# Performance work log

Measured on AMD Instinct MI355X. Metric: run time of the kernel, lower is better.

The kernel has to match this reference:

```python
import jax, jax.numpy as jnp
import numpy as np

N, D, H, K = 131072, 512, 128, 3
NPOS, NNEG = 8192, 8192
KM_ITERS = 4
PROTO_SHIFT = 0.15
PROTO_LOGIT_SCALE = 0.2
TEMP = 2.5


def _sq_cdist(x, c):
    # squared euclidean distance, matches torch.cdist(...).pow(2)
    d = jnp.sum(x * x, -1, keepdims=True) + jnp.sum(c * c, -1)[None, :] - 2.0 * (x @ c.T)
    return jnp.maximum(d, 0.0)


def _kmeans(x, k, iters):
    # torch.linspace(0, n-1, steps=k).long() init, fixed iteration count
    n = x.shape[0]
    idx = jnp.linspace(0.0, n - 1, k).astype(jnp.int32)
    centers = x[idx]
    for _ in range(iters):
        assign = jnp.argmin(_sq_cdist(x, centers), axis=1)
        sums = jax.ops.segment_sum(x, assign, num_segments=k)
        counts = jax.ops.segment_sum(jnp.ones((n,), x.dtype), assign, num_segments=k)[:, None]
        # empty cluster keeps old center (mask.any() branch in torch)
        centers = jnp.where(counts > 0, sums / jnp.maximum(counts, 1.0), centers)
    return centers


def setup_inputs() -> dict:
    key = jax.random.key(0)
    ks = jax.random.split(key, 10)
    s = 1.0 / np.sqrt(D).astype(np.float32)
    return {
        "z_cls": jax.random.normal(ks[0], (N, D), jnp.float32),
        "z_proto": jax.random.normal(ks[1], (N, D), jnp.float32),
        "pos_ctx": jax.random.normal(ks[2], (D,), jnp.float32),
        "neg_ctx": jax.random.normal(ks[3], (D,), jnp.float32),
        "W1": jax.random.normal(ks[4], (H, D), jnp.float32) * s,
        "b1": jnp.zeros((H,), jnp.float32),
        "W2": jax.random.normal(ks[5], (1, H), jnp.float32) * (1.0 / np.sqrt(H).astype(np.float32)),
        "b2": jnp.zeros((1,), jnp.float32),
        "Wp": jax.random.normal(ks[6], (D, D), jnp.float32) * s,
        "bp": jnp.zeros((D,), jnp.float32),
        "Wn": jax.random.normal(ks[7], (D, D), jnp.float32) * s,
        "bn": jnp.zeros((D,), jnp.float32),
        "pos_idx": jax.random.randint(ks[8], (NPOS,), 0, N),
        "neg_idx": jax.random.randint(ks[9], (NNEG,), 0, N),
    }


def reference(z_cls, z_proto, pos_ctx, neg_ctx, W1, b1, W2, b2, Wp, bp, Wn, bn, pos_idx, neg_idx):
    # _build_prototypes (pos_idx/neg_idx nonempty path)
    pos_proto = _kmeans(z_proto[pos_idx], K, KM_ITERS)          # [K, D]
    neg_proto = jnp.mean(z_proto[neg_idx], axis=0)              # [D]
    # _calibrate (ema not initialized -> no EMA blend)
    pos_proto = pos_proto + PROTO_SHIFT * (pos_ctx @ Wp.T + bp)[None, :]
    neg_proto = neg_proto + PROTO_SHIFT * (neg_ctx @ Wn.T + bn)
    # distances
    d_pos_all = _sq_cdist(z_proto, pos_proto)                   # [N, K]
    d_pos = jnp.min(d_pos_all, axis=1)
    pos_assign = jnp.argmin(d_pos_all, axis=1)
    d_neg = jnp.mean((z_proto - neg_proto[None, :]) ** 2, axis=1)
    proto_logit = (d_neg - d_pos) / np.sqrt(D).astype(np.float32)
    # cls head (eval mode: dropout is identity)
    h = jax.nn.relu(z_cls @ W1.T + b1)
    cls_logit = (h @ W2.T + b2)[:, 0]
    logits = (cls_logit + PROTO_LOGIT_SCALE * proto_logit) / TEMP
    prob = jax.nn.sigmoid(logits)
    return (logits, prob, PROTO_LOGIT_SCALE * proto_logit, pos_assign, d_pos_all, pos_proto, neg_proto)
```

## Files before the change

kernel.cpp:

```cpp
#include <hip/hip_runtime.h>
#include <hip/hip_bf16.h>

#define NPTS 131072
#define DIM  512
#define HID  128
#define KCL  3
#define NPOSI 8192
#define NNEGI 8192

typedef __attribute__((ext_vector_type(8))) short bf16x8;
typedef __attribute__((ext_vector_type(4))) float f32x4;

enum {
  WS_SHIFT_POS = 0,
  WS_SHIFT_NEG = 512,
  WS_NEGSUM    = 1024,
  WS_NEGPART   = 1536,
  WS_SUMS      = 132608,
  WS_PPROTO    = 138764,
  WS_PN        = 140812,
  WS_W1FRAG    = 140816,
  WS_CLSL      = 173584,
};
#define SUMS_STRIDE 1539

__device__ __forceinline__ short f2bf(float x) {
  __hip_bfloat16 h = __float2bfloat16(x);
  return *reinterpret_cast<short*>(&h);
}

__global__ __launch_bounds__(256) void k_prep(const float* __restrict__ W1,
                                              const float* __restrict__ Wp, const float* __restrict__ bp,
                                              const float* __restrict__ Wn, const float* __restrict__ bn,
                                              const float* __restrict__ pos_ctx, const float* __restrict__ neg_ctx,
                                              const float* __restrict__ zp, const int* __restrict__ neg_idx,
                                              float* __restrict__ ws) {
  int bid = blockIdx.x, t = threadIdx.x;
  if (bid < 32) {
    int fid = bid * 256 + t;
    int kc = fid >> 9;
    int n  = (fid >> 6) & 7;
    int l  = fid & 63;
    int row = n * 16 + (l & 15);
    int col = kc * 32 + (l >> 4) * 8;
    const float* src = W1 + (size_t)row * DIM + col;
    float4 v0 = *(const float4*)(src);
    float4 v1 = *(const float4*)(src + 4);
    bf16x8 f;
    f[0] = f2bf(v0.x); f[1] = f2bf(v0.y); f[2] = f2bf(v0.z); f[3] = f2bf(v0.w);
    f[4] = f2bf(v1.x); f[5] = f2bf(v1.y); f[6] = f2bf(v1.z); f[7] = f2bf(v1.w);
    ((bf16x8*)(ws + WS_W1FRAG))[fid] = f;
  } else if (bid < 64) {
    int b = bid - 32;
    int mat = b >> 4;
    const float* W    = mat ? Wn : Wp;
    const float* bias = mat ? bn : bp;
    const float* ctx  = mat ? neg_ctx : pos_ctx;
    float* outp = ws + (mat ? WS_SHIFT_NEG : WS_SHIFT_POS);
    int row = (b & 15) * 32 + (t >> 3);
    int sub = t & 7;
    const float* wr = W + row * DIM + sub * 64;
    const float* cr = ctx + sub * 64;
    float s = 0.f;
#pragma unroll
    for (int j = 0; j < 64; j += 4) {
      float4 w4 = *(const float4*)(wr + j);
      float4 c4 = *(const float4*)(cr + j);
      s += w4.x * c4.x + w4.y * c4.y + w4.z * c4.z + w4.w * c4.w;
    }
    s += __shfl_xor(s, 1);
    s += __shfl_xor(s, 2);
    s += __shfl_xor(s, 4);
    if (sub == 0) outp[row] = 0.15f * (s + bias[row]);
  } else if (bid < 320) {
    int jb = bid - 64;
    int c0 = t * 2;
    float a0 = 0.f, a1 = 0.f;
    int base = jb * 32;
#pragma unroll 4
    for (int jj = 0; jj < 32; ++jj) {
      int row = neg_idx[base + jj];
      float2 v = *(const float2*)(zp + (size_t)row * DIM + c0);
      a0 += v.x; a1 += v.y;
    }
    ws[WS_NEGPART + jb * DIM + c0]     = a0;
    ws[WS_NEGPART + jb * DIM + c0 + 1] = a1;
  } else {
    for (int idx = t; idx < 4 * SUMS_STRIDE; idx += 256) ws[WS_SUMS + idx] = 0.f;
  }
}

template <int IT>
__global__ __launch_bounds__(256) void k_km(const float* __restrict__ zp,
                                            const int* __restrict__ pos_idx,
                                            float* __restrict__ ws) {
  int bid = blockIdx.x, t = threadIdx.x;
  if (IT == 0 && bid == 256) {
    int c0 = t * 2;
    float a0 = 0.f, a1 = 0.f;
#pragma unroll 8
    for (int j = 0; j < 256; ++j) {
      float2 v = *(const float2*)(ws + WS_NEGPART + j * DIM + c0);
      a0 += v.x; a1 += v.y;
    }
    ws[WS_NEGSUM + c0]     = a0;
    ws[WS_NEGSUM + c0 + 1] = a1;
    return;
  }
  __shared__ float cc[KCL * DIM];
  __shared__ float cn[KCL];
  __shared__ float lsum[KCL * DIM];
  __shared__ float lcnt[KCL];
  int w = t >> 6, l = t & 63;

  for (int idx = t; idx < KCL * DIM; idx += 256) lsum[idx] = 0.f;
  if (t < KCL) lcnt[t] = 0.f;

  for (int idx = t; idx < KCL * DIM; idx += 256) {
    int k = idx >> 9;
    int sel = (k == 0) ? 0 : ((k == 1) ? 4095 : 8191);
    float v = zp[(size_t)pos_idx[sel] * DIM + (idx & 511)];
#pragma unroll
    for (int j = 0; j < IT; ++j) {
      float cntv = ws[WS_SUMS + j * SUMS_STRIDE + 3 * DIM + k];
      float sv   = ws[WS_SUMS + j * SUMS_STRIDE + idx];
      v = (cntv > 0.f) ? sv / cntv : v;
    }
    cc[idx] = v;
  }
  __syncthreads();
  if (w < KCL) {
    float s = 0.f;
#pragma unroll
    for (int m = 0; m < 8; ++m) { float v = cc[w * DIM + l + m * 64]; s += v * v; }
#pragma unroll
    for (int m = 1; m < 64; m <<= 1) s += __shfl_xor(s, m);
    if (l == 0) cn[w] = s;
  }
  __syncthreads();

  float ck0[8], ck1[8], ck2[8];
#pragma unroll
  for (int j = 0; j < 8; ++j) {
    ck0[j] = cc[0 * DIM + l * 8 + j];
    ck1[j] = cc[1 * DIM + l * 8 + j];
    ck2[j] = cc[2 * DIM + l * 8 + j];
  }
  float cn0 = cn[0], cn1 = cn[1], cn2 = cn[2];
  float acc0[8] = {0,0,0,0,0,0,0,0}, acc1[8] = {0,0,0,0,0,0,0,0}, acc2[8] = {0,0,0,0,0,0,0,0};
  float cnt0 = 0.f, cnt1 = 0.f, cnt2 = 0.f;

  int wid = bid * 4 + w;
#pragma unroll 2
  for (int p = wid; p < NPOSI; p += 1024) {
    int row = pos_idx[p];
    const float* xr = zp + (size_t)row * DIM + l * 8;
    float4 x0 = *(const float4*)(xr);
    float4 x1 = *(const float4*)(xr + 4);
    float x[8] = {x0.x, x0.y, x0.z, x0.w, x1.x, x1.y, x1.z, x1.w};
    float d0 = 0.f, d1 = 0.f, d2 = 0.f;
#pragma unroll
    for (int j = 0; j < 8; ++j) { d0 += x[j] * ck0[j]; d1 += x[j] * ck1[j]; d2 += x[j] * ck2[j]; }
#pragma unroll
    for (int m = 1; m < 64; m <<= 1) {
      d0 += __shfl_xor(d0, m); d1 += __shfl_xor(d1, m); d2 += __shfl_xor(d2, m);
    }
    float t0 = cn0 - 2.f * d0, t1 = cn1 - 2.f * d1, t2 = cn2 - 2.f * d2;
    int a = 0; float best = t0;
    if (t1 < best) { best = t1; a = 1; }
    if (t2 < best) { best = t2; a = 2; }
    if (a == 0)      { cnt0 += 1.f;
#pragma unroll
      for (int j = 0; j < 8; ++j) acc0[j] += x[j]; }
    else if (a == 1) { cnt1 += 1.f;
#pragma unroll
      for (int j = 0; j < 8; ++j) acc1[j] += x[j]; }
    else             { cnt2 += 1.f;
#pragma unroll
      for (int j = 0; j < 8; ++j) acc2[j] += x[j]; }
  }
#pragma unroll
  for (int j = 0; j < 8; ++j) {
    atomicAdd(&lsum[0 * DIM + l * 8 + j], acc0[j]);
    atomicAdd(&lsum[1 * DIM + l * 8 + j], acc1[j]);
    atomicAdd(&lsum[2 * DIM + l * 8 + j], acc2[j]);
  }
  if (l == 0) {
    atomicAdd(&lcnt[0], cnt0); atomicAdd(&lcnt[1], cnt1); atomicAdd(&lcnt[2], cnt2);
  }
  __syncthreads();
  for (int idx = t; idx < KCL * DIM; idx += 256) atomicAdd(&ws[WS_SUMS + IT * SUMS_STRIDE + idx], lsum[idx]);
  if (t < KCL) atomicAdd(&ws[WS_SUMS + IT * SUMS_STRIDE + 3 * DIM + t], lcnt[t]);
}

__global__ __launch_bounds__(256) void k_fin(const float* __restrict__ zp,
                                             const int* __restrict__ pos_idx,
                                             float* __restrict__ ws,
                                             float* __restrict__ out) {
  __shared__ __align__(16) float pp[4 * DIM];
  int t = threadIdx.x, w = t >> 6, l = t & 63;
  for (int idx = t; idx < KCL * DIM; idx += 256) {
    int k = idx >> 9, d = idx & 511;
    int sel = (k == 0) ? 0 : ((k == 1) ? 4095 : 8191);
    float v = zp[(size_t)pos_idx[sel] * DIM + d];
#pragma unroll
    for (int j = 0; j < 4; ++j) {
      float cntv = ws[WS_SUMS + j * SUMS_STRIDE + 3 * DIM + k];
      float sv   = ws[WS_SUMS + j * SUMS_STRIDE + idx];
      v = (cntv > 0.f) ? sv / cntv : v;
    }
    pp[idx] = v + ws[WS_SHIFT_POS + d];
  }
  for (int d = t; d < DIM; d += 256)
    pp[3 * DIM + d] = ws[WS_NEGSUM + d] * (1.f / NNEGI) + ws[WS_SHIFT_NEG + d];
  __syncthreads();
  {
    float s = 0.f;
#pragma unroll
    for (int m = 0; m < 8; ++m) { float v = pp[w * DIM + l + m * 64]; s += v * v; }
#pragma unroll
    for (int m = 1; m < 64; m <<= 1) s += __shfl_xor(s, m);
    if (l == 0) ws[WS_PN + w] = s;
  }
  for (int idx = t; idx < 4 * DIM; idx += 256) {
    ws[WS_PPROTO + idx] = pp[idx];
    out[7 * NPTS + idx] = pp[idx];
  }
}

__global__ __launch_bounds__(256, 2) void k_cls(const float* __restrict__ zc,
                                                const float* __restrict__ b1,
                                                const float* __restrict__ W2,
                                                const float* __restrict__ b2,
                                                float* __restrict__ ws) {
  int t = threadIdx.x, w = t >> 6, l = t & 63;
  int i0 = blockIdx.x * 64;
  const bf16x8* w1f = (const bf16x8*)(ws + WS_W1FRAG);
  int arow = i0 + w * 16 + (l & 15);
  const float* aptr = zc + (size_t)arow * DIM + (l >> 4) * 8;

  f32x4 acc[8];
#pragma unroll
  for (int n = 0; n < 8; ++n) acc[n] = (f32x4){0.f, 0.f, 0.f, 0.f};

  float4 A[3][2];
  bf16x8 B[2][8];
#pragma unroll
  for (int s = 0; s < 3; ++s) {
    A[s][0] = *(const float4*)(aptr + s * 32);
    A[s][1] = *(const float4*)(aptr + s * 32 + 4);
  }
#pragma unroll
  for (int n = 0; n < 8; ++n) B[0][n] = w1f[n * 64 + l];

#pragma unroll
  for (int kc = 0; kc < 16; ++kc) {
    float4 a0 = A[kc % 3][0], a1 = A[kc % 3][1];
    bf16x8 af;
    af[0] = f2bf(a0.x); af[1] = f2bf(a0.y); af[2] = f2bf(a0.z); af[3] = f2bf(a0.w);
    af[4] = f2bf(a1.x); af[5] = f2bf(a1.y); af[6] = f2bf(a1.z); af[7] = f2bf(a1.w);
    if (kc + 3 < 16) {
      A[kc % 3][0] = *(const float4*)(aptr + (kc + 3) * 32);
      A[kc % 3][1] = *(const float4*)(aptr + (kc + 3) * 32 + 4);
    }
    if (kc + 1 < 16) {
#pragma unroll
      for (int n = 0; n < 8; ++n) B[(kc + 1) & 1][n] = w1f[(kc + 1) * 512 + n * 64 + l];
    }
#pragma unroll
    for (int n = 0; n < 8; ++n)
      acc[n] = __builtin_amdgcn_mfma_f32_16x16x32_bf16(af, B[kc & 1][n], acc[n], 0, 0, 0);
  }

  float p[4] = {0.f, 0.f, 0.f, 0.f};
  int col_l = l & 15;
#pragma unroll
  for (int n = 0; n < 8; ++n) {
    int col = n * 16 + col_l;
    float bb = b1[col], w2v = W2[col];
#pragma unroll
    for (int r = 0; r < 4; ++r) {
      float h = acc[n][r] + bb;
      h = h > 0.f ? h : 0.f;
      p[r] += h * w2v;
    }
  }
#pragma unroll
  for (int m = 1; m < 16; m <<= 1) {
#pragma unroll
    for (int r = 0; r < 4; ++r) p[r] += __shfl_xor(p[r], m);
  }
  if (col_l == 0) {
    float b2v = b2[0];
    int rbase = i0 + w * 16 + (l >> 4) * 4;
#pragma unroll
    for (int r = 0; r < 4; ++r) ws[WS_CLSL + rbase + r] = p[r] + b2v;
  }
}

__global__ __launch_bounds__(256, 4) void k_proto(const float* __restrict__ zp,
                                                  const float* __restrict__ ws,
                                                  float* __restrict__ out) {
  __shared__ __align__(16) float pp[4 * DIM];
  __shared__ float pns[4];
  int t = threadIdx.x;
  for (int idx = t; idx < 4 * DIM; idx += 256) pp[idx] = ws[WS_PPROTO + idx];
  if (t < 4) pns[t] = ws[WS_PN + t];
  __syncthreads();

  int w = t >> 6, l = t & 63, s = l & 7, r = l >> 3;
  int i = blockIdx.x * 32 + w * 8 + r;
  const float* xr = zp + (size_t)i * DIM;

  float d0 = 0.f, d1 = 0.f, d2 = 0.f, dn = 0.f, sx = 0.f;
#pragma unroll
  for (int j = 0; j < 16; ++j) {
    int col = j * 32 + s * 4;
    float4 x  = *(const float4*)(xr + col);
    float4 c0 = *(const float4*)(&pp[0 * DIM + col]);
    float4 c1 = *(const float4*)(&pp[1 * DIM + col]);
    float4 c2 = *(const float4*)(&pp[2 * DIM + col]);
    float4 c3 = *(const float4*)(&pp[3 * DIM + col]);
    d0 += x.x * c0.x + x.y * c0.y + x.z * c0.z + x.w * c0.w;
    d1 += x.x * c1.x + x.y * c1.y + x.z * c1.z + x.w * c1.w;
    d2 += x.x * c2.x + x.y * c2.y + x.z * c2.z + x.w * c2.w;
    dn += x.x * c3.x + x.y * c3.y + x.z * c3.z + x.w * c3.w;
    sx += x.x * x.x  + x.y * x.y  + x.z * x.z  + x.w * x.w;
  }
#pragma unroll
  for (int m = 1; m < 8; m <<= 1) {
    d0 += __shfl_xor(d0, m);
    d1 += __shfl_xor(d1, m);
    d2 += __shfl_xor(d2, m);
    dn += __shfl_xor(dn, m);
    sx += __shfl_xor(sx, m);
  }
  if (s == 0) {
    float e0 = sx + pns[0] - 2.f * d0; e0 = fmaxf(e0, 0.f);
    float e1 = sx + pns[1] - 2.f * d1; e1 = fmaxf(e1, 0.f);
    float e2 = sx + pns[2] - 2.f * d2; e2 = fmaxf(e2, 0.f);
    float dpos = e0; int a = 0;
    if (e1 < dpos) { dpos = e1; a = 1; }
    if (e2 < dpos) { dpos = e2; a = 2; }
    float dneg = (sx + pns[3] - 2.f * dn) * (1.f / DIM);
    float plog = (dneg - dpos) * 0.04419417382415922f;
    float o2 = 0.2f * plog;
    float lg = (ws[WS_CLSL + i] + o2) * 0.4f;
    float prob = 1.f / (1.f + expf(-lg));
    out[i]            = lg;
    out[NPTS + i]     = prob;
    out[2 * NPTS + i] = o2;
    out[3 * NPTS + i] = (float)a;
    out[4 * NPTS + 3 * i]     = e0;
    out[4 * NPTS + 3 * i + 1] = e1;
    out[4 * NPTS + 3 * i + 2] = e2;
  }
}

extern "C" void kernel_launch(void* const* d_in, const int* in_sizes, int n_in,
                              void* d_out, int out_size, void* d_ws, size_t ws_size,
                              hipStream_t stream) {
  const float* z_cls   = (const float*)d_in[0];
  const float* z_proto = (const float*)d_in[1];
  const float* pos_ctx = (const float*)d_in[2];
  const float* neg_ctx = (const float*)d_in[3];
  const float* W1      = (const float*)d_in[4];
  const float* b1      = (const float*)d_in[5];
  const float* W2      = (const float*)d_in[6];
  const float* b2      = (const float*)d_in[7];
  const float* Wp      = (const float*)d_in[8];
  const float* bp      = (const float*)d_in[9];
  const float* Wn      = (const float*)d_in[10];
  const float* bn      = (const float*)d_in[11];
  const int* pos_idx   = (const int*)d_in[12];
  const int* neg_idx   = (const int*)d_in[13];
  float* out           = (float*)d_out;
  float* ws            = (float*)d_ws;

  k_prep<<<321, 256, 0, stream>>>(W1, Wp, bp, Wn, bn, pos_ctx, neg_ctx, z_proto, neg_idx, ws);
  k_km<0><<<257, 256, 0, stream>>>(z_proto, pos_idx, ws);
  k_km<1><<<256, 256, 0, stream>>>(z_proto, pos_idx, ws);
  k_km<2><<<256, 256, 0, stream>>>(z_proto, pos_idx, ws);
  k_km<3><<<256, 256, 0, stream>>>(z_proto, pos_idx, ws);
  k_fin<<<1, 256, 0, stream>>>(z_proto, pos_idx, ws, out);
  k_cls<<<NPTS / 64, 256, 0, stream>>>(z_cls, b1, W2, b2, ws);
  k_proto<<<NPTS / 32, 256, 0, stream>>>(z_proto, ws, out);
}
```

Baseline: 276.1 us.

## Fuse cls head with proto distances and pre-gather positive rows for kmeans

The cls MLP head and the prototype distance kernel are merged into one kernel. It stages z_cls and then z_proto tiles into LDS with async global-to-LDS loads and a swizzled layout, and keeps cls logits in shared memory instead of a workspace round trip. The positive-index rows are gathered once into a contiguous workspace buffer in the prep kernel, so each kmeans iteration reads them contiguously with 4 rows per wave over 512 blocks instead of doing indirect gathers. This removes a kernel launch and the cls-logit global traffic. In exchange it adds an extra 16 MB gather copy and a larger LDS footprint that may lower occupancy.

```diff
diff --git a/kernel.cpp b/kernel.cpp
--- a/kernel.cpp
+++ b/kernel.cpp
@@ -10,6 +10,9 @@
 
 typedef __attribute__((ext_vector_type(8))) short bf16x8;
 typedef __attribute__((ext_vector_type(4))) float f32x4;
+
+#define ASG __attribute__((address_space(1)))
+#define ASL __attribute__((address_space(3)))
 
 enum {
   WS_SHIFT_POS = 0,
@@ -20,7 +23,7 @@
   WS_PPROTO    = 138764,
   WS_PN        = 140812,
   WS_W1FRAG    = 140816,
-  WS_CLSL      = 173584,
+  WS_POSG      = 173584,
 };
 #define SUMS_STRIDE 1539
 
@@ -33,7 +36,8 @@
                                               const float* __restrict__ Wp, const float* __restrict__ bp,
                                               const float* __restrict__ Wn, const float* __restrict__ bn,
                                               const float* __restrict__ pos_ctx, const float* __restrict__ neg_ctx,
-                                              const float* __restrict__ zp, const int* __restrict__ neg_idx,
+                                              const float* __restrict__ zp,
+                                              const int* __restrict__ neg_idx, const int* __restrict__ pos_idx,
                                               float* __restrict__ ws) {
   int bid = blockIdx.x, t = threadIdx.x;
   if (bid < 32) {
@@ -77,7 +81,7 @@
     int c0 = t * 2;
     float a0 = 0.f, a1 = 0.f;
     int base = jb * 32;
-#pragma unroll 4
+#pragma unroll 8
     for (int jj = 0; jj < 32; ++jj) {
       int row = neg_idx[base + jj];
       float2 v = *(const float2*)(zp + (size_t)row * DIM + c0);
@@ -85,17 +89,35 @@
     }
     ws[WS_NEGPART + jb * DIM + c0]     = a0;
     ws[WS_NEGPART + jb * DIM + c0 + 1] = a1;
+  } else if (bid < 576) {
+    int j = bid - 320;
+    int w = t >> 6, l = t & 63;
+    int row0 = j * 32 + w * 8;
+#pragma unroll
+    for (int rb = 0; rb < 8; rb += 8) {
+      float4 a[8], b[8];
+#pragma unroll
+      for (int r = 0; r < 8; ++r) {
+        const float* src = zp + (size_t)pos_idx[row0 + rb + r] * DIM + l * 8;
+        a[r] = *(const float4*)(src);
+        b[r] = *(const float4*)(src + 4);
+      }
+#pragma unroll
+      for (int r = 0; r < 8; ++r) {
+        float* dst = ws + WS_POSG + (size_t)(row0 + rb + r) * DIM + l * 8;
+        *(float4*)(dst)     = a[r];
+        *(float4*)(dst + 4) = b[r];
+      }
+    }
   } else {
     for (int idx = t; idx < 4 * SUMS_STRIDE; idx += 256) ws[WS_SUMS + idx] = 0.f;
   }
 }
 
 template <int IT>
-__global__ __launch_bounds__(256) void k_km(const float* __restrict__ zp,
-                                            const int* __restrict__ pos_idx,
-                                            float* __restrict__ ws) {
+__global__ __launch_bounds__(256, 1) void k_km(float* __restrict__ ws) {
   int bid = blockIdx.x, t = threadIdx.x;
-  if (IT == 0 && bid == 256) {
+  if (IT == 0 && bid == 512) {
     int c0 = t * 2;
     float a0 = 0.f, a1 = 0.f;
 #pragma unroll 8
@@ -119,7 +141,7 @@
   for (int idx = t; idx < KCL * DIM; idx += 256) {
     int k = idx >> 9;
     int sel = (k == 0) ? 0 : ((k == 1) ? 4095 : 8191);
-    float v = zp[(size_t)pos_idx[sel] * DIM + (idx & 511)];
+    float v = ws[WS_POSG + (size_t)sel * DIM + (idx & 511)];
 #pragma unroll
     for (int j = 0; j < IT; ++j) {
       float cntv = ws[WS_SUMS + j * SUMS_STRIDE + 3 * DIM + k];
@@ -150,14 +172,17 @@
   float acc0[8] = {0,0,0,0,0,0,0,0}, acc1[8] = {0,0,0,0,0,0,0,0}, acc2[8] = {0,0,0,0,0,0,0,0};
   float cnt0 = 0.f, cnt1 = 0.f, cnt2 = 0.f;
 
-  int wid = bid * 4 + w;
-#pragma unroll 2
-  for (int p = wid; p < NPOSI; p += 1024) {
-    int row = pos_idx[p];
-    const float* xr = zp + (size_t)row * DIM + l * 8;
-    float4 x0 = *(const float4*)(xr);
-    float4 x1 = *(const float4*)(xr + 4);
-    float x[8] = {x0.x, x0.y, x0.z, x0.w, x1.x, x1.y, x1.z, x1.w};
+  int p0 = (bid * 4 + w) * 4;
+  const float* xbase = ws + WS_POSG + (size_t)p0 * DIM + l * 8;
+  float4 xa[4], xb[4];
+#pragma unroll
+  for (int r = 0; r < 4; ++r) {
+    xa[r] = *(const float4*)(xbase + r * DIM);
+    xb[r] = *(const float4*)(xbase + r * DIM + 4);
+  }
+#pragma unroll
+  for (int r = 0; r < 4; ++r) {
+    float x[8] = {xa[r].x, xa[r].y, xa[r].z, xa[r].w, xb[r].x, xb[r].y, xb[r].z, xb[r].w};
     float d0 = 0.f, d1 = 0.f, d2 = 0.f;
 #pragma unroll
     for (int j = 0; j < 8; ++j) { d0 += x[j] * ck0[j]; d1 += x[j] * ck1[j]; d2 += x[j] * ck2[j]; }
@@ -193,16 +218,13 @@
   if (t < KCL) atomicAdd(&ws[WS_SUMS + IT * SUMS_STRIDE + 3 * DIM + t], lcnt[t]);
 }
 
-__global__ __launch_bounds__(256) void k_fin(const float* __restrict__ zp,
-                                             const int* __restrict__ pos_idx,
-                                             float* __restrict__ ws,
-                                             float* __restrict__ out) {
+__global__ __launch_bounds__(256) void k_fin(float* __restrict__ ws, float* __restrict__ out) {
   __shared__ __align__(16) float pp[4 * DIM];
   int t = threadIdx.x, w = t >> 6, l = t & 63;
   for (int idx = t; idx < KCL * DIM; idx += 256) {
     int k = idx >> 9, d = idx & 511;
     int sel = (k == 0) ? 0 : ((k == 1) ? 4095 : 8191);
-    float v = zp[(size_t)pos_idx[sel] * DIM + d];
+    float v = ws[WS_POSG + (size_t)sel * DIM + d];
 #pragma unroll
     for (int j = 0; j < 4; ++j) {
       float cntv = ws[WS_SUMS + j * SUMS_STRIDE + 3 * DIM + k];
@@ -228,132 +250,169 @@
   }
 }
 
-__global__ __launch_bounds__(256, 2) void k_cls(const float* __restrict__ zc,
-                                                const float* __restrict__ b1,
-                                                const float* __restrict__ W2,
-                                                const float* __restrict__ b2,
-                                                float* __restrict__ ws) {
-  int t = threadIdx.x, w = t >> 6, l = t & 63;
-  int i0 = blockIdx.x * 64;
-  const bf16x8* w1f = (const bf16x8*)(ws + WS_W1FRAG);
-  int arow = i0 + w * 16 + (l & 15);
-  const float* aptr = zc + (size_t)arow * DIM + (l >> 4) * 8;
-
-  f32x4 acc[8];
-#pragma unroll
-  for (int n = 0; n < 8; ++n) acc[n] = (f32x4){0.f, 0.f, 0.f, 0.f};
-
-  float4 A[3][2];
-  bf16x8 B[2][8];
-#pragma unroll
-  for (int s = 0; s < 3; ++s) {
-    A[s][0] = *(const float4*)(aptr + s * 32);
-    A[s][1] = *(const float4*)(aptr + s * 32 + 4);
-  }
-#pragma unroll
-  for (int n = 0; n < 8; ++n) B[0][n] = w1f[n * 64 + l];
-
-#pragma unroll
-  for (int kc = 0; kc < 16; ++kc) {
-    float4 a0 = A[kc % 3][0], a1 = A[kc % 3][1];
-    bf16x8 af;
-    af[0] = f2bf(a0.x); af[1] = f2bf(a0.y); af[2] = f2bf(a0.z); af[3] = f2bf(a0.w);
-    af[4] = f2bf(a1.x); af[5] = f2bf(a1.y); af[6] = f2bf(a1.z); af[7] = f2bf(a1.w);
-    if (kc + 3 < 16) {
-      A[kc % 3][0] = *(const float4*)(aptr + (kc + 3) * 32);
-      A[kc % 3][1] = *(const float4*)(aptr + (kc + 3) * 32 + 4);
-    }
-    if (kc + 1 < 16) {
-#pragma unroll
-      for (int n = 0; n < 8; ++n) B[(kc + 1) & 1][n] = w1f[(kc + 1) * 512 + n * 64 + l];
-    }
-#pragma unroll
-    for (int n = 0; n < 8; ++n)
-      acc[n] = __builtin_amdgcn_mfma_f32_16x16x32_bf16(af, B[kc & 1][n], acc[n], 0, 0, 0);
-  }
-
-  float p[4] = {0.f, 0.f, 0.f, 0.f};
-  int col_l = l & 15;
-#pragma unroll
-  for (int n = 0; n < 8; ++n) {
-    int col = n * 16 + col_l;
-    float bb = b1[col], w2v = W2[col];
-#pragma unroll
-    for (int r = 0; r < 4; ++r) {
-      float h = acc[n][r] + bb;
-      h = h > 0.f ? h : 0.f;
-      p[r] += h * w2v;
-    }
-  }
-#pragma unroll
-  for (int m = 1; m < 16; m <<= 1) {
-#pragma unroll
-    for (int r = 0; r < 4; ++r) p[r] += __shfl_xor(p[r], m);
-  }
-  if (col_l == 0) {
-    float b2v = b2[0];
-    int rbase = i0 + w * 16 + (l >> 4) * 4;
-#pragma unroll
-    for (int r = 0; r < 4; ++r) ws[WS_CLSL + rbase + r] = p[r] + b2v;
-  }
-}
-
-__global__ __launch_bounds__(256, 4) void k_proto(const float* __restrict__ zp,
+__global__ __launch_bounds__(256, 2) void k_fused(const float* __restrict__ zc,
+                                                  const float* __restrict__ zp,
+                                                  const float* __restrict__ b1,
+                                                  const float* __restrict__ W2,
+                                                  const float* __restrict__ b2,
                                                   const float* __restrict__ ws,
                                                   float* __restrict__ out) {
+  __shared__ __align__(16) float Ast[2][16 * DIM];
   __shared__ __align__(16) float pp[4 * DIM];
   __shared__ float pns[4];
-  int t = threadIdx.x;
+  __shared__ float clsv[32];
+
+  int t = threadIdx.x, w = t >> 6, l = t & 63;
+  int pr = w >> 1, hw = w & 1;
+  int i0 = blockIdx.x * 32;
+  int pairRow0 = i0 + pr * 16;
+
+  if (t < 32) clsv[t] = 0.f;
+
+  {
+    const float* gsrc = zc + (size_t)(pairRow0 + hw * 8) * DIM;
+    float* ldsb = &Ast[pr][0];
+#pragma unroll
+    for (int i = 0; i < 16; ++i) {
+      int rloc = hw * 8 + (i >> 1);
+      int c = ((i & 1) * 256) + ((l * 4) ^ ((rloc & 7) << 3));
+      const float* src = gsrc + (size_t)(i >> 1) * DIM + c;
+      float* dst = ldsb + rloc * DIM + (i & 1) * 256;
+      __builtin_amdgcn_global_load_lds((const ASG void*)src, (ASL void*)dst, 16, 0, 0);
+    }
+  }
+
   for (int idx = t; idx < 4 * DIM; idx += 256) pp[idx] = ws[WS_PPROTO + idx];
   if (t < 4) pns[t] = ws[WS_PN + t];
-  __syncthreads();
-
-  int w = t >> 6, l = t & 63, s = l & 7, r = l >> 3;
-  int i = blockIdx.x * 32 + w * 8 + r;
-  const float* xr = zp + (size_t)i * DIM;
-
-  float d0 = 0.f, d1 = 0.f, d2 = 0.f, dn = 0.f, sx = 0.f;
-#pragma unroll
-  for (int j = 0; j < 16; ++j) {
-    int col = j * 32 + s * 4;
-    float4 x  = *(const float4*)(xr + col);
-    float4 c0 = *(const float4*)(&pp[0 * DIM + col]);
-    float4 c1 = *(const float4*)(&pp[1 * DIM + col]);
-    float4 c2 = *(const float4*)(&pp[2 * DIM + col]);
-    float4 c3 = *(const float4*)(&pp[3 * DIM + col]);
-    d0 += x.x * c0.x + x.y * c0.y + x.z * c0.z + x.w * c0.w;
-    d1 += x.x * c1.x + x.y * c1.y + x.z * c1.z + x.w * c1.w;
-    d2 += x.x * c2.x + x.y * c2.y + x.z * c2.z + x.w * c2.w;
-    dn += x.x * c3.x + x.y * c3.y + x.z * c3.z + x.w * c3.w;
-    sx += x.x * x.x  + x.y * x.y  + x.z * x.z  + x.w * x.w;
-  }
-#pragma unroll
-  for (int m = 1; m < 8; m <<= 1) {
-    d0 += __shfl_xor(d0, m);
-    d1 += __shfl_xor(d1, m);
-    d2 += __shfl_xor(d2, m);
-    dn += __shfl_xor(dn, m);
-    sx += __shfl_xor(sx, m);
-  }
-  if (s == 0) {
-    float e0 = sx + pns[0] - 2.f * d0; e0 = fmaxf(e0, 0.f);
-    float e1 = sx + pns[1] - 2.f * d1; e1 = fmaxf(e1, 0.f);
-    float e2 = sx + pns[2] - 2.f * d2; e2 = fmaxf(e2, 0.f);
-    float dpos = e0; int a = 0;
-    if (e1 < dpos) { dpos = e1; a = 1; }
-    if (e2 < dpos) { dpos = e2; a = 2; }
-    float dneg = (sx + pns[3] - 2.f * dn) * (1.f / DIM);
-    float plog = (dneg - dpos) * 0.04419417382415922f;
-    float o2 = 0.2f * plog;
-    float lg = (ws[WS_CLSL + i] + o2) * 0.4f;
-    float prob = 1.f / (1.f + expf(-lg));
-    out[i]            = lg;
-    out[NPTS + i]     = prob;
-    out[2 * NPTS + i] = o2;
-    out[3 * NPTS + i] = (float)a;
-    out[4 * NPTS + 3 * i]     = e0;
-    out[4 * NPTS + 3 * i + 1] = e1;
-    out[4 * NPTS + 3 * i + 2] = e2;
+  int col_l = l & 15;
+  float b1c[4], w2c[4];
+#pragma unroll
+  for (int nn = 0; nn < 4; ++nn) {
+    int col = (hw * 4 + nn) * 16 + col_l;
+    b1c[nn] = b1[col];
+    w2c[nn] = W2[col];
+  }
+  float b2v = b2[0];
+  __syncthreads();
+
+  {
+    const bf16x8* w1f = (const bf16x8*)(ws + WS_W1FRAG);
+    const float* pl = &Ast[pr][0];
+    int sub = l >> 4, row = l & 15;
+    int swz = (row & 7) << 3;
+    int abase = row * DIM;
+    f32x4 acc[4];
+#pragma unroll
+    for (int nn = 0; nn < 4; ++nn) acc[nn] = (f32x4){0.f, 0.f, 0.f, 0.f};
+    bf16x8 B2[2][4];
+#pragma unroll
+    for (int nn = 0; nn < 4; ++nn) B2[0][nn] = w1f[(hw * 4 + nn) * 64 + l];
+
+#pragma unroll
+    for (int kc = 0; kc < 16; ++kc) {
+      int pidx = abase + ((kc * 32 + sub * 8) ^ swz);
+      float4 a0 = *(const float4*)&pl[pidx];
+      float4 a1 = *(const float4*)&pl[pidx + 4];
+      if (kc < 15) {
+#pragma unroll
+        for (int nn = 0; nn < 4; ++nn)
+          B2[(kc + 1) & 1][nn] = w1f[(kc + 1) * 512 + (hw * 4 + nn) * 64 + l];
+      }
+      bf16x8 af;
+      af[0] = f2bf(a0.x); af[1] = f2bf(a0.y); af[2] = f2bf(a0.z); af[3] = f2bf(a0.w);
+      af[4] = f2bf(a1.x); af[5] = f2bf(a1.y); af[6] = f2bf(a1.z); af[7] = f2bf(a1.w);
+#pragma unroll
+      for (int nn = 0; nn < 4; ++nn)
+        acc[nn] = __builtin_amdgcn_mfma_f32_16x16x32_bf16(af, B2[kc & 1][nn], acc[nn], 0, 0, 0);
+    }
+    float prt[4] = {0.f, 0.f, 0.f, 0.f};
+#pragma unroll
+    for (int nn = 0; nn < 4; ++nn) {
+#pragma unroll
+      for (int r = 0; r < 4; ++r) {
+        float h = acc[nn][r] + b1c[nn];
+        h = h > 0.f ? h : 0.f;
+        prt[r] += h * w2c[nn];
+      }
+    }
+#pragma unroll
+    for (int m = 1; m < 16; m <<= 1) {
+#pragma unroll
+      for (int r = 0; r < 4; ++r) prt[r] += __shfl_xor(prt[r], m);
+    }
+    if (col_l == 0) {
+      float add = hw ? 0.f : b2v;
+#pragma unroll
+      for (int r = 0; r < 4; ++r)
+        atomicAdd(&clsv[pr * 16 + sub * 4 + r], prt[r] + add);
+    }
+  }
+  __syncthreads();
+
+  {
+    const float* gsrc = zp + (size_t)(pairRow0 + hw * 8) * DIM;
+    float* ldsb = &Ast[pr][0];
+#pragma unroll
+    for (int i = 0; i < 16; ++i) {
+      int rloc = hw * 8 + (i >> 1);
+      int c = ((i & 1) * 256) + ((l * 4) ^ ((rloc & 7) << 3));
+      const float* src = gsrc + (size_t)(i >> 1) * DIM + c;
+      float* dst = ldsb + rloc * DIM + (i & 1) * 256;
+      __builtin_amdgcn_global_load_lds((const ASG void*)src, (ASL void*)dst, 16, 0, 0);
+    }
+  }
+  __syncthreads();
+
+  {
+    int s = l & 7, r8 = l >> 3;
+    const float* xl = &Ast[w >> 1][0];
+    int rloc = (w & 1) * 8 + r8;
+    int swz = (rloc & 7) << 3;
+    int xbase = rloc * DIM;
+    float d0 = 0.f, d1 = 0.f, d2 = 0.f, dn = 0.f, sx = 0.f;
+#pragma unroll
+    for (int j = 0; j < 16; ++j) {
+      int c = s * 64 + j * 4;
+      float4 x  = *(const float4*)&xl[xbase + (c ^ swz)];
+      float4 c0 = *(const float4*)&pp[0 * DIM + c];
+      float4 c1 = *(const float4*)&pp[1 * DIM + c];
+      float4 c2 = *(const float4*)&pp[2 * DIM + c];
+      float4 c3 = *(const float4*)&pp[3 * DIM + c];
+      d0 += x.x * c0.x + x.y * c0.y + x.z * c0.z + x.w * c0.w;
+      d1 += x.x * c1.x + x.y * c1.y + x.z * c1.z + x.w * c1.w;
+      d2 += x.x * c2.x + x.y * c2.y + x.z * c2.z + x.w * c2.w;
+      dn += x.x * c3.x + x.y * c3.y + x.z * c3.z + x.w * c3.w;
+      sx += x.x * x.x  + x.y * x.y  + x.z * x.z  + x.w * x.w;
+    }
+#pragma unroll
+    for (int m = 1; m < 8; m <<= 1) {
+      d0 += __shfl_xor(d0, m);
+      d1 += __shfl_xor(d1, m);
+      d2 += __shfl_xor(d2, m);
+      dn += __shfl_xor(dn, m);
+      sx += __shfl_xor(sx, m);
+    }
+    if (s == 0) {
+      int i = i0 + w * 8 + r8;
+      float e0 = sx + pns[0] - 2.f * d0; e0 = fmaxf(e0, 0.f);
+      float e1 = sx + pns[1] - 2.f * d1; e1 = fmaxf(e1, 0.f);
+      float e2 = sx + pns[2] - 2.f * d2; e2 = fmaxf(e2, 0.f);
+      float dpos = e0; int a = 0;
+      if (e1 < dpos) { dpos = e1; a = 1; }
+      if (e2 < dpos) { dpos = e2; a = 2; }
+      float dneg = (sx + pns[3] - 2.f * dn) * (1.f / DIM);
+      float plog = (dneg - dpos) * 0.04419417382415922f;
+      float o2 = 0.2f * plog;
+      float lg = (clsv[w * 8 + r8] + o2) * 0.4f;
+      float prob = 1.f / (1.f + expf(-lg));
+      out[i]            = lg;
+      out[NPTS + i]     = prob;
+      out[2 * NPTS + i] = o2;
+      out[3 * NPTS + i] = (float)a;
+      out[4 * NPTS + 3 * i]     = e0;
+      out[4 * NPTS + 3 * i + 1] = e1;
+      out[4 * NPTS + 3 * i + 2] = e2;
+    }
   }
 }
 
@@ -377,12 +436,11 @@
   float* out           = (float*)d_out;
   float* ws            = (float*)d_ws;
 
-  k_prep<<<321, 256, 0, stream>>>(W1, Wp, bp, Wn, bn, pos_ctx, neg_ctx, z_proto, neg_idx, ws);
-  k_km<0><<<257, 256, 0, stream>>>(z_proto, pos_idx, ws);
-  k_km<1><<<256, 256, 0, stream>>>(z_proto, pos_idx, ws);
-  k_km<2><<<256, 256, 0, stream>>>(z_proto, pos_idx, ws);
-  k_km<3><<<256, 256, 0, stream>>>(z_proto, pos_idx, ws);
-  k_fin<<<1, 256, 0, stream>>>(z_proto, pos_idx, ws, out);
-  k_cls<<<NPTS / 64, 256, 0, stream>>>(z_cls, b1, W2, b2, ws);
-  k_proto<<<NPTS / 32, 256, 0, stream>>>(z_proto, ws, out);
-}
+  k_prep<<<577, 256, 0, stream>>>(W1, Wp, bp, Wn, bn, pos_ctx, neg_ctx, z_proto, neg_idx, pos_idx, ws);
+  k_km<0><<<513, 256, 0, stream>>>(ws);
+  k_km<1><<<512, 256, 0, stream>>>(ws);
+  k_km<2><<<512, 256, 0, stream>>>(ws);
+  k_km<3><<<512, 256, 0, stream>>>(ws);
+  k_fin<<<1, 256, 0, stream>>>(ws, out);
+  k_fused<<<NPTS / 32, 256, 0, stream>>>(z_cls, z_proto, b1, W2, b2, ws, out);
+}
```

Result: slower. 314.1 us (+13.8%).
